# Performance work log

Hardware: AMD Instinct MI355X
Metric: run time of the kernel (lower is better)

## Reference

```python
import jax, jax.numpy as jnp
import numpy as np

GROUP_SIZE = 16
MIN_SIGMA = 1e-4


def setup_inputs() -> dict:
    key = jax.random.key(0)
    k1, k2, k3 = jax.random.split(key, 3)
    B, N, M, F = 4, 8192, 4096, 64
    return {
        "point_cloud": jax.random.normal(k1, (B, 3, N), dtype=jnp.float32),
        "query_cloud": jax.random.normal(k2, (B, 3, M), dtype=jnp.float32),
        "point_features": jax.random.normal(k3, (B, F, N), dtype=jnp.float32),
        "temperature": jnp.asarray(1.0, dtype=jnp.float32),
    }


def reference(point_cloud, query_cloud, point_features, temperature):
    # point_cloud: (B,3,N), query_cloud: (B,3,M), point_features: (B,F,N)
    k = GROUP_SIZE
    # Pairwise squared distances (B, M, N): ||q||^2 + ||p||^2 - 2 q.p
    q_sq = jnp.sum(query_cloud ** 2, axis=1)              # (B, M)
    p_sq = jnp.sum(point_cloud ** 2, axis=1)              # (B, N)
    qp = jnp.einsum('bdm,bdn->bmn', query_cloud, point_cloud)
    d2 = q_sq[:, :, None] + p_sq[:, None, :] - 2.0 * qp   # (B, M, N)
    # k nearest neighbors per query
    _, idx = jax.lax.top_k(-d2, k)                         # (B, M, k)

    # Gather neighbor coords and features: (B, 3, M, k), (B, F, M, k)
    idx_b = idx[:, None, :, :]                             # (B,1,M,k)
    grouped_points = jnp.take_along_axis(
        point_cloud[:, :, None, :], jnp.broadcast_to(idx_b, (idx.shape[0], 3, idx.shape[1], k)), axis=3)
    grouped_features = jnp.take_along_axis(
        point_features[:, :, None, :],
        jnp.broadcast_to(idx_b, (idx.shape[0], point_features.shape[1], idx.shape[1], k)), axis=3)

    # Soft-projection weights
    sigma = jnp.maximum(temperature ** 2, jnp.asarray(MIN_SIGMA, dtype=temperature.dtype))
    deltas = grouped_points - query_cloud[:, :, :, None]   # (B,3,M,k)
    dist = jnp.sum(deltas ** 2, axis=1, keepdims=True) / sigma  # (B,1,M,k)
    weights = jax.nn.softmax(-dist, axis=3)                # (B,1,M,k)

    projected_points = jnp.sum(grouped_points * weights, axis=3)     # (B,3,M)
    propagated_features = jnp.sum(grouped_features * weights, axis=3)  # (B,F,M)
    return (projected_points, propagated_features)
```

## Files before the change

### kernel.cpp

```cpp
#include <hip/hip_runtime.h>


#define BB 4
#define NN 8192
#define MM 4096
#define FF 64
#define KK 16
#define CHUNK 1024
#define NCHUNK 8
#define QPW 4
#define QPB 32
#define SCAP 54
#define NTHR 1024
#define STG 33

__device__ __forceinline__ void gload_lds16(const float* g, float* l) {
    __builtin_amdgcn_global_load_lds(
        (const __attribute__((address_space(1))) void*)g,
        (__attribute__((address_space(3))) void*)l, 16, 0, 0);
}

__device__ __forceinline__ float min3f(float a, float b, float c) {
    float d;
    asm("v_min3_f32 %0, %1, %2, %3" : "=v"(d) : "v"(a), "v"(b), "v"(c));
    return d;
}

__global__ __launch_bounds__(256) void prep_kernel(const float* __restrict__ pf,
                                                   float* __restrict__ pfT,
                                                   const float* __restrict__ pc,
                                                   float* __restrict__ pc4,
                                                   int doT, int doPS) {
    const int b = blockIdx.y;
    const int n0 = blockIdx.x * 64;
    const int t = threadIdx.x;
    if (doPS && t < 64) {
        int n = n0 + t;
        const float* s = pc + (size_t)b * 3 * NN;
        float x = s[n], y = s[NN + n], z = s[2 * NN + n];
        float ps = fmaf(x, x, fmaf(y, y, z * z));
        float* d = pc4 + (size_t)b * 4 * NN;
        d[n] = x;
        d[NN + n] = y;
        d[2 * NN + n] = z;
        d[3 * NN + n] = ps;
    }
    if (!doT) return;
    __shared__ float tile[64][65];
    const int n = t & 63, fq = t >> 6;
#pragma unroll
    for (int i = 0; i < 16; ++i) {
        int f = fq * 16 + i;
        tile[f][n] = pf[(size_t)b * FF * NN + (size_t)f * NN + n0 + n];
    }
    __syncthreads();
    const int f2 = t & 63, nq = t >> 6;
#pragma unroll
    for (int i = 0; i < 16; ++i) {
        int nn2 = nq * 16 + i;
        pfT[(size_t)b * NN * FF + (size_t)(n0 + nn2) * FF + f2] = tile[f2][nn2];
    }
}

__device__ __forceinline__ unsigned mapf(float f) {
    unsigned u = __float_as_uint(f);
    return (u & 0x80000000u) ? ~u : (u | 0x80000000u);
}
__device__ __forceinline__ float unmapf(unsigned k) {
    return (k & 0x80000000u) ? __uint_as_float(k ^ 0x80000000u)
                             : __uint_as_float(~k);
}

#define ISSUE(C, BUF)                                                       \
    do {                                                                    \
        if (usePS) {                                                        \
            int pl_ = t >> 8;                                               \
            int ii_ = (t & 255) * 4;                                        \
            gload_lds16(pc4b + pl_ * NN + (C)*CHUNK + ii_,                  \
                        s_pts + (BUF) * (4 * CHUNK) + pl_ * CHUNK + ii_);   \
        } else if (t < 256) {                                               \
            int base_ = (C)*CHUNK + t * 4;                                  \
            float4 x4_ = *(const float4*)(pcb + base_);                     \
            float4 y4_ = *(const float4*)(pcb + NN + base_);                \
            float4 z4_ = *(const float4*)(pcb + 2 * NN + base_);            \
            float* bp_ = s_pts + (BUF) * (4 * CHUNK);                       \
            *(float4*)(bp_ + t * 4) = x4_;                                  \
            *(float4*)(bp_ + CHUNK + t * 4) = y4_;                          \
            *(float4*)(bp_ + 2 * CHUNK + t * 4) = z4_;                      \
            float4 p4_;                                                     \
            p4_.x = fmaf(x4_.x, x4_.x, fmaf(y4_.x, y4_.x, z4_.x * z4_.x));  \
            p4_.y = fmaf(x4_.y, x4_.y, fmaf(y4_.y, y4_.y, z4_.y * z4_.y));  \
            p4_.z = fmaf(x4_.z, x4_.z, fmaf(y4_.z, y4_.z, z4_.z * z4_.z));  \
            p4_.w = fmaf(x4_.w, x4_.w, fmaf(y4_.w, y4_.w, z4_.w * z4_.w));  \
            *(float4*)(bp_ + 3 * CHUNK + t * 4) = p4_;                      \
        }                                                                   \
    } while (0)

#define VAL(X, Y, Z, PS, Q) \
    fmaf((X), qx2[Q], fmaf((Y), qy2[Q], fmaf((Z), qz2[Q], (PS))))

#define PUSH(WQ, V, I)                                          \
    do {                                                        \
        int pos_ = atomicAdd(&s_cnt[WQ], 1);                    \
        if (pos_ < SCAP) {                                      \
            s_surv[((WQ)*SCAP + pos_) * 2] = (V);               \
            s_surv[((WQ)*SCAP + pos_) * 2 + 1] = __int_as_float(I); \
        }                                                       \
    } while (0)

__global__ __launch_bounds__(NTHR, 8) void soft_proj_kernel(
    const float* __restrict__ pc, const float* __restrict__ qc,
    const float* __restrict__ pf, const float* __restrict__ pfT,
    const float* __restrict__ pc4g, const float* __restrict__ temp,
    float* __restrict__ out, int useT, int usePS) {
    __shared__ __align__(16) float s_pts[2 * 4 * CHUNK];
    __shared__ __align__(16) float s_surv[QPB * SCAP * 2];
    __shared__ int s_cnt[QPB];
    __shared__ int s_sel[QPB * KK];
    __shared__ float s_thr[2 * QPB];

    const int bid = blockIdx.x;
    const int b = bid >> 7;
    const int m0 = (bid & 127) * QPB;
    const int t = threadIdx.x;
    const int wave = t >> 6;
    const int lane = t & 63;
    const int pairIdx = wave & 7;
    const int half = wave >> 3;

    const float* pcb = pc + (size_t)b * 3 * NN;
    const float* qcb = qc + (size_t)b * 3 * MM;
    const float* pc4b = pc4g + (size_t)b * 4 * NN;

    float qx2[QPW], qy2[QPW], qz2[QPW];
#pragma unroll
    for (int q = 0; q < QPW; ++q) {
        int m = m0 + pairIdx * QPW + q;
        qx2[q] = -2.0f * qcb[m];
        qy2[q] = -2.0f * qcb[MM + m];
        qz2[q] = -2.0f * qcb[2 * MM + m];
    }

    float mnA[QPW], mnB[QPW];
#pragma unroll
    for (int q = 0; q < QPW; ++q) { mnA[q] = 3.0e38f; mnB[q] = 3.0e38f; }

    ISSUE(0, 0);
    __syncthreads();
    for (int c = 0; c < NCHUNK; ++c) {
        if (c + 1 < NCHUNK) ISSUE(c + 1, (c + 1) & 1);
        const float* bp = s_pts + (c & 1) * (4 * CHUNK);
        const int ob = half * 512 + lane * 4;
#pragma unroll
        for (int g = 0; g < 2; ++g) {
            int oo = ob + g * 256;
            float4 x4 = *(const float4*)(bp + oo);
            float4 y4 = *(const float4*)(bp + CHUNK + oo);
            float4 z4 = *(const float4*)(bp + 2 * CHUNK + oo);
            float4 p4 = *(const float4*)(bp + 3 * CHUNK + oo);
#pragma unroll
            for (int q = 0; q < QPW; ++q) {
                float v0 = VAL(x4.x, y4.x, z4.x, p4.x, q);
                float v1 = VAL(x4.y, y4.y, z4.y, p4.y, q);
                float v2 = VAL(x4.z, y4.z, z4.z, p4.z, q);
                float v3 = VAL(x4.w, y4.w, z4.w, p4.w, q);
                mnA[q] = min3f(v0, v1, mnA[q]);
                mnB[q] = min3f(v2, v3, mnB[q]);
            }
        }
        __syncthreads();
    }

    float thrv[QPW];
#pragma unroll
    for (int q = 0; q < QPW; ++q) {
        unsigned key = mapf(fminf(mnA[q], mnB[q]));
        unsigned res = 0u;
        for (int bb = 31; bb >= 16; --bb) {
            unsigned cand = res | (1u << bb);
            unsigned long long bal = __ballot(key < cand);
            int c2 = __popcll(bal);
            if (c2 < 8) res = cand;
        }
        thrv[q] = unmapf(res | 0xFFFFu);
    }
    if (lane == 0) {
#pragma unroll
        for (int q = 0; q < QPW; ++q)
            s_thr[half * QPB + pairIdx * QPW + q] = thrv[q];
    }
    if (t < QPB) s_cnt[t] = 0;
    __syncthreads();
#pragma unroll
    for (int q = 0; q < QPW; ++q)
        thrv[q] = fmaxf(s_thr[pairIdx * QPW + q], s_thr[QPB + pairIdx * QPW + q]);

    ISSUE(0, 0);
    __syncthreads();
    for (int c = 0; c < NCHUNK; ++c) {
        if (c + 1 < NCHUNK) ISSUE(c + 1, (c + 1) & 1);
        const float* bp = s_pts + (c & 1) * (4 * CHUNK);
        const int ob = half * 512 + lane * 4;
#pragma unroll
        for (int g = 0; g < 2; ++g) {
            int oo = ob + g * 256;
            float4 x4 = *(const float4*)(bp + oo);
            float4 y4 = *(const float4*)(bp + CHUNK + oo);
            float4 z4 = *(const float4*)(bp + 2 * CHUNK + oo);
            float4 p4 = *(const float4*)(bp + 3 * CHUNK + oo);
            int gi = c * CHUNK + oo;
#pragma unroll
            for (int q = 0; q < QPW; ++q) {
                float v0 = VAL(x4.x, y4.x, z4.x, p4.x, q);
                float v1 = VAL(x4.y, y4.y, z4.y, p4.y, q);
                float v2 = VAL(x4.z, y4.z, z4.z, p4.z, q);
                float v3 = VAL(x4.w, y4.w, z4.w, p4.w, q);
                if (fminf(min3f(v0, v1, v2), v3) <= thrv[q]) {
                    int wqq = pairIdx * QPW + q;
                    if (v0 <= thrv[q]) PUSH(wqq, v0, gi + 0);
                    if (v1 <= thrv[q]) PUSH(wqq, v1, gi + 1);
                    if (v2 <= thrv[q]) PUSH(wqq, v2, gi + 2);
                    if (v3 <= thrv[q]) PUSH(wqq, v3, gi + 3);
                }
            }
        }
        __syncthreads();
    }

#pragma unroll
    for (int qq = 0; qq < 2; ++qq) {
        int wq = wave * 2 + qq;
        int cnt = s_cnt[wq];
        cnt = __builtin_amdgcn_readfirstlane(cnt);
        if (cnt > SCAP) cnt = SCAP;
        bool valid = lane < cnt;
        float mv = 0.f;
        int mi = 0;
        if (valid) {
            mv = s_surv[(wq * SCAP + lane) * 2];
            mi = __float_as_int(s_surv[(wq * SCAP + lane) * 2 + 1]);
        }
        int rank = 0;
        for (int j = 0; j < cnt; ++j) {
            float vj = s_surv[(wq * SCAP + j) * 2];
            int ij = __float_as_int(s_surv[(wq * SCAP + j) * 2 + 1]);
            if (valid && (vj < mv || (vj == mv && ij < mi))) rank++;
        }
        if (valid && rank < KK) s_sel[wq * KK + rank] = mi;
    }
    __syncthreads();

    float* stage = s_surv;
    float tval = temp[0];
    float sigma = fmaxf(tval * tval, 1.0e-4f);
    float inv_sigma = 1.0f / sigma;
    const float* pfTb = pfT + (size_t)b * NN * FF;
    const float* pfb = pf + (size_t)b * FF * NN;

#pragma unroll
    for (int qq = 0; qq < 2; ++qq) {
        int wq = wave * 2 + qq;
        int m = m0 + wq;
        float qxe = qcb[m], qye = qcb[MM + m], qze = qcb[2 * MM + m];
        int ik[KK];
        float dk[KK];
#pragma unroll
        for (int k = 0; k < KK; ++k) {
            int ii = __builtin_amdgcn_readfirstlane(s_sel[wq * KK + k]);
            ik[k] = ii;
            float px = pcb[ii], py = pcb[NN + ii], pz = pcb[2 * NN + ii];
            float dx = px - qxe, dy = py - qye, dz = pz - qze;
            dk[k] = fmaf(dx, dx, fmaf(dy, dy, dz * dz));
        }
        float dmin = dk[0];
#pragma unroll
        for (int k = 1; k < KK; ++k) dmin = fminf(dmin, dk[k]);
        float ssum = 0.f, facc = 0.f, sx = 0.f, sy = 0.f, sz = 0.f;
#pragma unroll
        for (int k = 0; k < KK; ++k) {
            float e = __expf((dmin - dk[k]) * inv_sigma);
            ssum += e;
            float px = pcb[ik[k]], py = pcb[NN + ik[k]], pz = pcb[2 * NN + ik[k]];
            sx = fmaf(e, px, sx);
            sy = fmaf(e, py, sy);
            sz = fmaf(e, pz, sz);
            float fv = useT ? pfTb[(size_t)ik[k] * FF + lane]
                            : pfb[(size_t)lane * NN + ik[k]];
            facc = fmaf(e, fv, facc);
        }
        float rs = 1.0f / ssum;
        stage[lane * STG + wq] = facc * rs;
        if (lane == 0) {
            stage[(64) * STG + wq] = sx * rs;
            stage[(65) * STG + wq] = sy * rs;
            stage[(66) * STG + wq] = sz * rs;
        }
    }
    __syncthreads();

    const size_t featOff = (size_t)BB * 3 * MM;
    for (int j = t; j < 67 * QPB; j += NTHR) {
        int row = j >> 5, col = j & 31;
        float v = stage[row * STG + col];
        int m = m0 + col;
        if (row < 64)
            out[featOff + (size_t)b * FF * MM + (size_t)row * MM + m] = v;
        else
            out[(size_t)b * 3 * MM + (size_t)(row - 64) * MM + m] = v;
    }
}

extern "C" void kernel_launch(void* const* d_in, const int* in_sizes, int n_in,
                              void* d_out, int out_size, void* d_ws, size_t ws_size,
                              hipStream_t stream) {
    (void)in_sizes; (void)n_in; (void)out_size;
    const float* pc = (const float*)d_in[0];
    const float* qc = (const float*)d_in[1];
    const float* pf = (const float*)d_in[2];
    const float* temp = (const float*)d_in[3];
    float* out = (float*)d_out;
    float* pfT = (float*)d_ws;
    const size_t needT = (size_t)BB * NN * FF * sizeof(float);
    const size_t needPS = (size_t)BB * 4 * NN * sizeof(float);
    int useT = (ws_size >= needT && d_ws != nullptr) ? 1 : 0;
    int usePS = (ws_size >= needT + needPS && d_ws != nullptr) ? 1 : 0;
    float* pc4 = (float*)((char*)d_ws + needT);

    if (useT || usePS) {
        hipLaunchKernelGGL(prep_kernel, dim3(NN / 64, BB), dim3(256), 0, stream,
                           pf, pfT, pc, pc4, useT, usePS);
    }
    hipLaunchKernelGGL(soft_proj_kernel, dim3((BB * MM) / QPB), dim3(NTHR), 0,
                       stream, pc, qc, pf, pfT, pc4, temp, out, useT, usePS);
}
```

Before: 122.5 us.

## Stream point coordinates directly from global memory instead of LDS double buffering

Both kNN scan passes now read point coordinates (and precomputed squared norms) straight from global memory with float4 loads. This replaces the chunked LDS double buffer and its per-chunk block barriers, and the partitioning changes so each half-block scans a contiguous half of the points. It frees 32 KB of LDS and removes 16 block-wide syncs, which could help occupancy. The survivor capacity also grows. In exchange, every wave re-reads the point data from global or L2 instead of sharing one staged copy, which adds cache traffic and load latency.

New measurement: 125.4 us. 2.4% more time.

```diff
diff --git a/kernel.cpp b/kernel.cpp
--- a/kernel.cpp
+++ b/kernel.cpp
@@ -6,19 +6,11 @@
 #define MM 4096
 #define FF 64
 #define KK 16
-#define CHUNK 1024
-#define NCHUNK 8
 #define QPW 4
 #define QPB 32
-#define SCAP 54
+#define SCAP 64
 #define NTHR 1024
 #define STG 33
-
-__device__ __forceinline__ void gload_lds16(const float* g, float* l) {
-    __builtin_amdgcn_global_load_lds(
-        (const __attribute__((address_space(1))) void*)g,
-        (__attribute__((address_space(3))) void*)l, 16, 0, 0);
-}
 
 __device__ __forceinline__ float min3f(float a, float b, float c) {
     float d;
@@ -71,31 +63,6 @@
                              : __uint_as_float(~k);
 }
 
-#define ISSUE(C, BUF)                                                       \
-    do {                                                                    \
-        if (usePS) {                                                        \
-            int pl_ = t >> 8;                                               \
-            int ii_ = (t & 255) * 4;                                        \
-            gload_lds16(pc4b + pl_ * NN + (C)*CHUNK + ii_,                  \
-                        s_pts + (BUF) * (4 * CHUNK) + pl_ * CHUNK + ii_);   \
-        } else if (t < 256) {                                               \
-            int base_ = (C)*CHUNK + t * 4;                                  \
-            float4 x4_ = *(const float4*)(pcb + base_);                     \
-            float4 y4_ = *(const float4*)(pcb + NN + base_);                \
-            float4 z4_ = *(const float4*)(pcb + 2 * NN + base_);            \
-            float* bp_ = s_pts + (BUF) * (4 * CHUNK);                       \
-            *(float4*)(bp_ + t * 4) = x4_;                                  \
-            *(float4*)(bp_ + CHUNK + t * 4) = y4_;                          \
-            *(float4*)(bp_ + 2 * CHUNK + t * 4) = z4_;                      \
-            float4 p4_;                                                     \
-            p4_.x = fmaf(x4_.x, x4_.x, fmaf(y4_.x, y4_.x, z4_.x * z4_.x));  \
-            p4_.y = fmaf(x4_.y, x4_.y, fmaf(y4_.y, y4_.y, z4_.y * z4_.y));  \
-            p4_.z = fmaf(x4_.z, x4_.z, fmaf(y4_.z, y4_.z, z4_.z * z4_.z));  \
-            p4_.w = fmaf(x4_.w, x4_.w, fmaf(y4_.w, y4_.w, z4_.w * z4_.w));  \
-            *(float4*)(bp_ + 3 * CHUNK + t * 4) = p4_;                      \
-        }                                                                   \
-    } while (0)
-
 #define VAL(X, Y, Z, PS, Q) \
     fmaf((X), qx2[Q], fmaf((Y), qy2[Q], fmaf((Z), qz2[Q], (PS))))
 
@@ -108,12 +75,25 @@
         }                                                       \
     } while (0)
 
+#define LOADG(OO)                                                           \
+    float4 x4 = *(const float4*)(base + (OO));                              \
+    float4 y4 = *(const float4*)(base + NN + (OO));                         \
+    float4 z4 = *(const float4*)(base + 2 * NN + (OO));                     \
+    float4 p4;                                                              \
+    if (usePS) {                                                            \
+        p4 = *(const float4*)(base + 3 * NN + (OO));                        \
+    } else {                                                                \
+        p4.x = fmaf(x4.x, x4.x, fmaf(y4.x, y4.x, z4.x * z4.x));            \
+        p4.y = fmaf(x4.y, x4.y, fmaf(y4.y, y4.y, z4.y * z4.y));            \
+        p4.z = fmaf(x4.z, x4.z, fmaf(y4.z, y4.z, z4.z * z4.z));            \
+        p4.w = fmaf(x4.w, x4.w, fmaf(y4.w, y4.w, z4.w * z4.w));            \
+    }
+
 __global__ __launch_bounds__(NTHR, 8) void soft_proj_kernel(
     const float* __restrict__ pc, const float* __restrict__ qc,
     const float* __restrict__ pf, const float* __restrict__ pfT,
     const float* __restrict__ pc4g, const float* __restrict__ temp,
     float* __restrict__ out, int useT, int usePS) {
-    __shared__ __align__(16) float s_pts[2 * 4 * CHUNK];
     __shared__ __align__(16) float s_surv[QPB * SCAP * 2];
     __shared__ int s_cnt[QPB];
     __shared__ int s_sel[QPB * KK];
@@ -130,7 +110,7 @@
 
     const float* pcb = pc + (size_t)b * 3 * NN;
     const float* qcb = qc + (size_t)b * 3 * MM;
-    const float* pc4b = pc4g + (size_t)b * 4 * NN;
+    const float* base = usePS ? pc4g + (size_t)b * 4 * NN : pcb;
 
     float qx2[QPW], qy2[QPW], qz2[QPW];
 #pragma unroll
@@ -145,19 +125,12 @@
 #pragma unroll
     for (int q = 0; q < QPW; ++q) { mnA[q] = 3.0e38f; mnB[q] = 3.0e38f; }
 
-    ISSUE(0, 0);
-    __syncthreads();
-    for (int c = 0; c < NCHUNK; ++c) {
-        if (c + 1 < NCHUNK) ISSUE(c + 1, (c + 1) & 1);
-        const float* bp = s_pts + (c & 1) * (4 * CHUNK);
-        const int ob = half * 512 + lane * 4;
-#pragma unroll
-        for (int g = 0; g < 2; ++g) {
-            int oo = ob + g * 256;
-            float4 x4 = *(const float4*)(bp + oo);
-            float4 y4 = *(const float4*)(bp + CHUNK + oo);
-            float4 z4 = *(const float4*)(bp + 2 * CHUNK + oo);
-            float4 p4 = *(const float4*)(bp + 3 * CHUNK + oo);
+    {
+        const int ob = half * 4096 + lane * 4;
+#pragma unroll 2
+        for (int it = 0; it < 16; ++it) {
+            int oo = ob + it * 256;
+            LOADG(oo);
 #pragma unroll
             for (int q = 0; q < QPW; ++q) {
                 float v0 = VAL(x4.x, y4.x, z4.x, p4.x, q);
@@ -168,7 +141,6 @@
                 mnB[q] = min3f(v2, v3, mnB[q]);
             }
         }
-        __syncthreads();
     }
 
     float thrv[QPW];
@@ -195,20 +167,12 @@
     for (int q = 0; q < QPW; ++q)
         thrv[q] = fmaxf(s_thr[pairIdx * QPW + q], s_thr[QPB + pairIdx * QPW + q]);
 
-    ISSUE(0, 0);
-    __syncthreads();
-    for (int c = 0; c < NCHUNK; ++c) {
-        if (c + 1 < NCHUNK) ISSUE(c + 1, (c + 1) & 1);
-        const float* bp = s_pts + (c & 1) * (4 * CHUNK);
-        const int ob = half * 512 + lane * 4;
-#pragma unroll
-        for (int g = 0; g < 2; ++g) {
-            int oo = ob + g * 256;
-            float4 x4 = *(const float4*)(bp + oo);
-            float4 y4 = *(const float4*)(bp + CHUNK + oo);
-            float4 z4 = *(const float4*)(bp + 2 * CHUNK + oo);
-            float4 p4 = *(const float4*)(bp + 3 * CHUNK + oo);
-            int gi = c * CHUNK + oo;
+    {
+        const int ob = half * 4096 + lane * 4;
+#pragma unroll 2
+        for (int it = 0; it < 16; ++it) {
+            int oo = ob + it * 256;
+            LOADG(oo);
 #pragma unroll
             for (int q = 0; q < QPW; ++q) {
                 float v0 = VAL(x4.x, y4.x, z4.x, p4.x, q);
@@ -217,15 +181,15 @@
                 float v3 = VAL(x4.w, y4.w, z4.w, p4.w, q);
                 if (fminf(min3f(v0, v1, v2), v3) <= thrv[q]) {
                     int wqq = pairIdx * QPW + q;
-                    if (v0 <= thrv[q]) PUSH(wqq, v0, gi + 0);
-                    if (v1 <= thrv[q]) PUSH(wqq, v1, gi + 1);
-                    if (v2 <= thrv[q]) PUSH(wqq, v2, gi + 2);
-                    if (v3 <= thrv[q]) PUSH(wqq, v3, gi + 3);
+                    if (v0 <= thrv[q]) PUSH(wqq, v0, oo + 0);
+                    if (v1 <= thrv[q]) PUSH(wqq, v1, oo + 1);
+                    if (v2 <= thrv[q]) PUSH(wqq, v2, oo + 2);
+                    if (v3 <= thrv[q]) PUSH(wqq, v3, oo + 3);
                 }
             }
         }
-        __syncthreads();
-    }
+    }
+    __syncthreads();
 
 #pragma unroll
     for (int qq = 0; qq < 2; ++qq) {
```
